# Kernel tuning notes

Hardware: AMD Instinct MI355X
Metric: run time of the kernel (lower is better)

## Reference

```python
import jax, jax.numpy as jnp
import numpy as np

RADIUS = 10  # watermark_radius
EPS = 1e-5   # BatchNorm eps

def _conv(x, w, b, g, be, m, v):
    # Conv2d 3x3 pad 1 + BatchNorm(eval) + ReLU, NCHW
    y = jax.lax.conv_general_dilated(x, w, (1, 1), 'SAME',
                                     dimension_numbers=('NCHW', 'OIHW', 'NCHW'))
    y = y + b[None, :, None, None]
    y = g[None, :, None, None] * (y - m[None, :, None, None]) * jax.lax.rsqrt(v + EPS)[None, :, None, None] + be[None, :, None, None]
    return jax.nn.relu(y)

def _watermark_indices(C, H, W, L, r):
    # Replicates the (channel, i, j) iteration order of the torch loop.
    chs, ys, xs = [], [], []
    cy0, cx0 = H // 2, W // 2
    for c in range(C):
        for i in range(-r, r + 1):
            for j in range(-r, r + 1):
                if len(chs) >= L:
                    return np.array(chs), np.array(ys), np.array(xs)
                y, x = cy0 + i, cx0 + j
                if 0 <= y < H and 0 <= x < W and i * i + j * j <= r * r:
                    chs.append(c); ys.append(y); xs.append(x)
    return np.array(chs), np.array(ys), np.array(xs)

def setup_inputs() -> dict:
    key = jax.random.key(0)
    ks = jax.random.split(key, 8)
    B, Cc, H, W, L = 16, 64, 256, 256, 256
    s = 0.05  # weight scale for numerical stability
    inp = {
        'image': jax.random.normal(ks[0], (B, 3, H, W), jnp.float32),
        'message': jax.random.uniform(ks[1], (B, L), jnp.float32),
        'w0': jax.random.normal(ks[2], (Cc, 3, 3, 3), jnp.float32) * s,
        'b0': jnp.zeros((Cc,), jnp.float32),
        'g0': jnp.ones((Cc,), jnp.float32),
        'be0': jnp.zeros((Cc,), jnp.float32),
        'm0': jnp.zeros((Cc,), jnp.float32),
        'v0': jnp.ones((Cc,), jnp.float32),
        'wk': jax.random.normal(ks[3], (3, Cc, Cc, 3, 3), jnp.float32) * s,
        'bk': jnp.zeros((3, Cc), jnp.float32),
        'gk': jnp.ones((3, Cc), jnp.float32),
        'bek': jnp.zeros((3, Cc), jnp.float32),
        'mk': jnp.zeros((3, Cc), jnp.float32),
        'vk': jnp.ones((3, Cc), jnp.float32),
        'wa': jax.random.normal(ks[4], (Cc, Cc + 3 + L, 3, 3), jnp.float32) * s,
        'ba': jnp.zeros((Cc,), jnp.float32),
        'ga': jnp.ones((Cc,), jnp.float32),
        'bea': jnp.zeros((Cc,), jnp.float32),
        'ma': jnp.zeros((Cc,), jnp.float32),
        'va': jnp.ones((Cc,), jnp.float32),
        'wf': jax.random.normal(ks[5], (3, Cc, 1, 1), jnp.float32) * s,
        'bf': jnp.zeros((3,), jnp.float32),
    }
    return inp

def reference(image, message, w0, b0, g0, be0, m0, v0,
              wk, bk, gk, bek, mk, vk,
              wa, ba, ga, bea, ma, va, wf, bf):
    B, _, H, W = image.shape
    L = message.shape[1]
    # conv stack
    x = _conv(image, w0, b0, g0, be0, m0, v0)
    for t in range(wk.shape[0]):
        x = _conv(x, wk[t], bk[t], gk[t], bek[t], mk[t], vk[t])
    C = x.shape[1]
    # FFT2 over spatial dims
    fft = jnp.fft.fft2(x.astype(jnp.complex64))
    # vectorized tree-ring watermark scatter (precomputed static indices)
    ch, yy, xx = _watermark_indices(C, H, W, L, RADIUS)
    vals = message[:, :ch.shape[0]]                      # [B, L]
    cvals = (vals + 1j * vals).astype(jnp.complex64)     # complex(value, value)
    fft = fft.at[:, ch, yy, xx].set(cvals)
    enc = jnp.fft.ifft2(fft).real.astype(image.dtype)
    # concat [expanded message, encoded, image]
    msg = jnp.broadcast_to(message[:, :, None, None], (B, L, H, W))
    cat = jnp.concatenate([msg, enc, image], axis=1)
    y = _conv(cat, wa, ba, ga, bea, ma, va)
    # final 1x1 conv
    out = jnp.einsum('bchw,oc->bohw', y, wf[:, :, 0, 0]) + bf[None, :, None, None]
    return out
```

## Files before the change

kernel.cpp:

```cpp
#include <hip/hip_runtime.h>
#include <hip/hip_bf16.h>

#define HH 256
#define WW 256
#define NB 16
#define CC 64
#define NL 256
#define HWSZ (HH*WW)
#define EPSV 1e-5f
#define CAST 104
#define NYK 16
#define YK0 118

using bf16 = __hip_bfloat16;
using short8  = __attribute__((ext_vector_type(8))) short;
using floatx4 = __attribute__((ext_vector_type(4))) float;

__device__ __forceinline__ ushort f2b(float f){
    bf16 h = __float2bfloat16(f);
    union { bf16 h; ushort u; } cv; cv.h = h; return cv.u;
}
__device__ __forceinline__ float b2fu(ushort u){
    union { unsigned int i; float f; } cv; cv.i = ((unsigned int)u) << 16; return cv.f;
}

__global__ void prep_w_k(const float* __restrict__ wk, const float* __restrict__ wa,
                         ushort* __restrict__ wkb2, ushort* __restrict__ wab2)
{
    int i = blockIdx.x*256 + threadIdx.x;
    const int NWK = 3*9*64*64, NWA = 9*64*96;
    if (i < NWK) {
        int ci8 = i & 7; int r = i >> 3;
        int lane = r & 63; r >>= 6;
        int mi = r & 3; r >>= 2;
        int g = r % 18; int t = r / 18;
        int q = g / 6, kc2 = (g / 3) & 1, p = g % 3;
        int quad = lane >> 4, n16 = lane & 15;
        int co = mi*16 + n16, ci = kc2*32 + quad*8 + ci8, tap = p*3 + q;
        wkb2[i] = f2b(wk[(((size_t)t*64 + co)*64 + ci)*9 + tap]);
    } else if (i < NWK + NWA) {
        int i2 = i - NWK;
        int ci8 = i2 & 7; int r = i2 >> 3;
        int lane = r & 63; r >>= 6;
        int mi = r & 3; r >>= 2;
        int g = r;
        int q = g / 9, kc3 = (g / 3) % 3, p = g % 3;
        int quad = lane >> 4, n16 = lane & 15;
        int co = mi*16 + n16, ci = kc3*32 + quad*8 + ci8, tap = p*3 + q;
        float v = 0.f;
        if (ci < 64)      v = wa[((size_t)co*323 + 256 + ci)*9 + tap];
        else if (ci < 67) v = wa[((size_t)co*323 + 320 + (ci-64))*9 + tap];
        wab2[i2] = f2b(v);
    }
}

#define LDAF(DST, G) { const ushort* bp = wbase + (size_t)(G)*2048;            \
    _Pragma("unroll") for (int mi_=0; mi_<4; mi_++)                            \
        DST[mi_] = *(const short8*)(bp + mi_*512); }

#define MFMA_GRP(AF, BF, P)                                                    \
    _Pragma("unroll") for (int mi_=0; mi_<4; mi_++) {                          \
      _Pragma("unroll") for (int ni_=0; ni_<4; ni_++)                          \
        acc[mi_][ni_] = __builtin_amdgcn_mfma_f32_16x16x32_bf16(               \
            AF[mi_], BF[ni_+(P)], acc[mi_][ni_], 0, 0, 0); }

__global__ __launch_bounds__(256) void conv0_k(
    const float* __restrict__ img, const float* __restrict__ w0,
    const float* __restrict__ bias, const float* __restrict__ gamma,
    const float* __restrict__ beta, const float* __restrict__ mean,
    const float* __restrict__ var, ushort* __restrict__ outp)
{
    __shared__ float s_i[3][18][18];
    __shared__ float s_wv[64*27];
    __shared__ float s_al[64], s_be[64];
    __shared__ ushort __align__(16) s_y[256*72];

    int tid = threadIdx.x;
    int x0 = blockIdx.x*16, y0 = blockIdx.y*16, b = blockIdx.z;
    if (tid < 64) {
        float a = gamma[tid]*rsqrtf(var[tid]+EPSV);
        s_al[tid] = a; s_be[tid] = (bias[tid]-mean[tid])*a + beta[tid];
    }
    for (int c = tid; c < 64*27; c += 256) s_wv[c] = w0[c];
    for (int c = tid; c < 3*18*18; c += 256) {
        int ci = c / 324, pp = c % 324, py = pp/18, px = pp%18;
        int gy = y0-1+py, gx = x0-1+px;
        float v = 0.f;
        if ((unsigned)gy < 256u && (unsigned)gx < 256u)
            v = img[((size_t)b*3 + ci)*HWSZ + gy*256 + gx];
        s_i[ci][py][px] = v;
    }
    __syncthreads();

    int ly = tid >> 4, lx = tid & 15;
    float xv[27];
    #pragma unroll
    for (int ci=0;ci<3;ci++)
      #pragma unroll
      for (int p=0;p<3;p++)
        #pragma unroll
        for (int q=0;q<3;q++)
            xv[ci*9+p*3+q] = s_i[ci][ly+p][lx+q];

    for (int co=0; co<64; co++) {
        float a = 0.f;
        #pragma unroll
        for (int j=0;j<27;j++) a += xv[j]*s_wv[co*27+j];
        s_y[tid*72 + co] = f2b(fmaxf(s_al[co]*a + s_be[co], 0.f));
    }
    __syncthreads();
    size_t obase = (size_t)b*HWSZ*64;
    for (int c = tid; c < 256*8; c += 256) {
        int ci8 = c & 7, px = c >> 3;
        int gy = y0 + (px>>4), gx = x0 + (px&15);
        *(uint4*)&outp[obase + (size_t)(gy*256+gx)*64 + ci8*8] =
            *(const uint4*)&s_y[px*72 + ci8*8];
    }
}

__global__ __launch_bounds__(256,3) void convm_k(
    const ushort* __restrict__ in, const ushort* __restrict__ wgt,
    ushort* __restrict__ outp,
    const float* __restrict__ gamma, const float* __restrict__ beta,
    const float* __restrict__ mean,  const float* __restrict__ var,
    const float* __restrict__ bias,  float* __restrict__ plane)
{
    __shared__ ushort __align__(16) s_x[18*18*72];
    __shared__ float s_al[64], s_be[64];

    const int tid = threadIdx.x;
    const int x0 = blockIdx.x*16, y0 = blockIdx.y*16, b = blockIdx.z;

    if (tid < 64) {
        float a = gamma[tid]*rsqrtf(var[tid]+EPSV);
        s_al[tid] = a; s_be[tid] = (bias[tid]-mean[tid])*a + beta[tid];
    }
    const size_t ibase = (size_t)b*HWSZ*64;
    for (int c = tid; c < 18*18*8; c += 256) {
        int ci8 = c & 7, pp = c >> 3;
        int px = pp % 18, py = pp / 18;
        int gy = y0-1+py, gx = x0-1+px;
        uint4 v = make_uint4(0,0,0,0);
        if ((unsigned)gy < 256u && (unsigned)gx < 256u)
            v = *(const uint4*)&in[ibase + (size_t)(gy*256+gx)*64 + ci8*8];
        *(uint4*)&s_x[(py*18+px)*72 + ci8*8] = v;
    }
    __syncthreads();

    const int lane = tid & 63, wid = tid >> 6;
    const int n16 = lane & 15, quad = lane >> 4;
    const ushort* wbase = wgt + (size_t)lane*8;

    floatx4 acc[4][4];
    #pragma unroll
    for (int mi=0;mi<4;mi++)
      #pragma unroll
      for (int ni=0;ni<4;ni++)
        #pragma unroll
        for (int r=0;r<4;r++) acc[mi][ni][r] = 0.f;

    short8 afA[4], afB[4], bfA[6], bfB[6];

    LDAF(afA, 0);
    #pragma unroll
    for (int rr=0; rr<6; rr++)
        bfA[rr] = *(const short8*)&s_x[((wid*4+rr)*18 + n16)*72 + quad*8];

    #pragma unroll
    for (int g=0; g<18; g++) {
        const int p = g % 3, j = g / 3;
        if (g+1 < 18) {
            if (g & 1) { LDAF(afA, g+1); } else { LDAF(afB, g+1); }
        }
        if (p == 0 && j+1 < 6) {
            const int nq = (j+1) >> 1, nk = (j+1) & 1;
            if (j & 1) {
                #pragma unroll
                for (int rr=0; rr<6; rr++)
                    bfA[rr] = *(const short8*)&s_x[((wid*4+rr)*18 + n16 + nq)*72 + nk*32 + quad*8];
            } else {
                #pragma unroll
                for (int rr=0; rr<6; rr++)
                    bfB[rr] = *(const short8*)&s_x[((wid*4+rr)*18 + n16 + nq)*72 + nk*32 + quad*8];
            }
        }
        if (g & 1) { if (j & 1) { MFMA_GRP(afB, bfB, p) } else { MFMA_GRP(afB, bfA, p) } }
        else       { if (j & 1) { MFMA_GRP(afA, bfB, p) } else { MFMA_GRP(afA, bfA, p) } }
    }
    __syncthreads();

    ushort* s_y = s_x;
    #pragma unroll
    for (int mi=0;mi<4;mi++)
      #pragma unroll
      for (int ni=0;ni<4;ni++) {
        int px = (wid*4+ni)*16 + n16;
        int cob = mi*16 + quad*4;
        ushort u[4];
        #pragma unroll
        for (int r=0;r<4;r++) {
            float y = fmaxf(s_al[cob+r]*acc[mi][ni][r] + s_be[cob+r], 0.f);
            u[r] = f2b(y);
            if (plane && mi==0 && quad==0 && r==0)
                plane[(size_t)b*HWSZ + (y0+wid*4+ni)*256 + x0 + n16] = y;
        }
        uint2 pk; pk.x = (uint)u[0] | ((uint)u[1]<<16); pk.y = (uint)u[2] | ((uint)u[3]<<16);
        *(uint2*)&s_y[px*72 + cob] = pk;
      }
    __syncthreads();
    for (int c = tid; c < 256*8; c += 256) {
        int ci8 = c & 7, px = c >> 3;
        int gy = y0 + (px>>4), gx = x0 + (px&15);
        *(uint4*)&outp[ibase + (size_t)(gy*256+gx)*64 + ci8*8] =
            *(const uint4*)&s_y[px*72 + ci8*8];
    }
}

__global__ __launch_bounds__(256,2) void conva_k(
    const ushort* __restrict__ enc, const float* __restrict__ img,
    const float* __restrict__ dplane, const ushort* __restrict__ wgt,
    const float* __restrict__ gamma, const float* __restrict__ beta,
    const float* __restrict__ mean,  const float* __restrict__ var,
    const float* __restrict__ bias,
    const float* __restrict__ Tb,
    const float* __restrict__ wf, const float* __restrict__ bfv,
    float* __restrict__ outp)
{
    __shared__ ushort __align__(16) s_x[18*18*CAST];
    __shared__ float s_al[64], s_be[64];
    __shared__ float s_T[64*9];
    __shared__ float s_wf[3*64];
    __shared__ float s_bf[3];

    const int tid = threadIdx.x;
    const int x0 = blockIdx.x*16, y0 = blockIdx.y*16, b = blockIdx.z;

    if (tid < 64) {
        float a = gamma[tid]*rsqrtf(var[tid]+EPSV);
        s_al[tid] = a; s_be[tid] = (bias[tid]-mean[tid])*a + beta[tid];
    }
    if (tid < 192) s_wf[tid] = wf[tid];
    if (tid < 3)   s_bf[tid] = bfv[tid];
    for (int c = tid; c < 64*9; c += 256) s_T[c] = Tb[(size_t)b*576 + c];

    const size_t ibase = (size_t)b*HWSZ*64;
    for (int c = tid; c < 18*18*8; c += 256) {
        int ci8 = c & 7, pp = c >> 3;
        int px = pp % 18, py = pp / 18;
        int gy = y0-1+py, gx = x0-1+px;
        uint4 v = make_uint4(0,0,0,0);
        if ((unsigned)gy < 256u && (unsigned)gx < 256u) {
            v = *(const uint4*)&enc[ibase + (size_t)(gy*256+gx)*64 + ci8*8];
            if (ci8 == 0) {
                float d = dplane[(size_t)b*HWSZ + gy*256 + gx];
                ushort nb = f2b(b2fu((ushort)(v.x & 0xffffu)) + d);
                v.x = (v.x & 0xffff0000u) | (uint)nb;
            }
        }
        *(uint4*)&s_x[(py*18+px)*CAST + ci8*8] = v;
    }
    for (int c = tid; c < 18*18*5; c += 256) {
        int ci8 = 8 + c % 5, pp = c / 5;
        int px = pp % 18, py = pp / 18;
        int gy = y0-1+py, gx = x0-1+px;
        uint4 v = make_uint4(0,0,0,0);
        if (ci8 == 8 && (unsigned)gy < 256u && (unsigned)gx < 256u) {
            float i0 = img[((size_t)b*3 + 0)*HWSZ + gy*256 + gx];
            float i1 = img[((size_t)b*3 + 1)*HWSZ + gy*256 + gx];
            float i2 = img[((size_t)b*3 + 2)*HWSZ + gy*256 + gx];
            v.x = (uint)f2b(i0) | ((uint)f2b(i1) << 16);
            v.y = (uint)f2b(i2);
        }
        *(uint4*)&s_x[(py*18+px)*CAST + ci8*8] = v;
    }
    __syncthreads();

    const int lane = tid & 63, wid = tid >> 6;
    const int n16 = lane & 15, quad = lane >> 4;
    const ushort* wbase = wgt + (size_t)lane*8;

    floatx4 acc[4][4];
    #pragma unroll
    for (int mi=0;mi<4;mi++)
      #pragma unroll
      for (int ni=0;ni<4;ni++)
        #pragma unroll
        for (int r=0;r<4;r++) acc[mi][ni][r] = 0.f;

    short8 afA[4], afB[4], bfA[6], bfB[6];

    LDAF(afA, 0);
    #pragma unroll
    for (int rr=0; rr<6; rr++)
        bfA[rr] = *(const short8*)&s_x[((wid*4+rr)*18 + n16)*CAST + quad*8];

    #pragma unroll
    for (int g=0; g<27; g++) {
        const int p = g % 3, j = g / 3;
        if (g+1 < 27) {
            if (g & 1) { LDAF(afA, g+1); } else { LDAF(afB, g+1); }
        }
        if (p == 0 && j+1 < 9) {
            const int nq = (j+1) / 3, nk = (j+1) % 3;
            if (j & 1) {
                #pragma unroll
                for (int rr=0; rr<6; rr++)
                    bfA[rr] = *(const short8*)&s_x[((wid*4+rr)*18 + n16 + nq)*CAST + nk*32 + quad*8];
            } else {
                #pragma unroll
                for (int rr=0; rr<6; rr++)
                    bfB[rr] = *(const short8*)&s_x[((wid*4+rr)*18 + n16 + nq)*CAST + nk*32 + quad*8];
            }
        }
        if (g & 1) { if (j & 1) { MFMA_GRP(afB, bfB, p) } else { MFMA_GRP(afB, bfA, p) } }
        else       { if (j & 1) { MFMA_GRP(afA, bfB, p) } else { MFMA_GRP(afA, bfA, p) } }
    }

    float po[3][4];
    #pragma unroll
    for (int o=0;o<3;o++)
      #pragma unroll
      for (int ni=0;ni<4;ni++) po[o][ni] = 0.f;

    #pragma unroll
    for (int mi=0;mi<4;mi++) {
        int cob = mi*16 + quad*4;
        #pragma unroll
        for (int r=0;r<4;r++) {
            int co = cob + r;
            float al = s_al[co], be = s_be[co];
            const float* t = &s_T[co*9];
            float w0f = s_wf[0*64+co], w1f = s_wf[1*64+co], w2f = s_wf[2*64+co];
            #pragma unroll
            for (int ni=0;ni<4;ni++) {
                int h = y0 + wid*4 + ni, w = x0 + n16;
                float tv = t[0];
                if (h==0)   tv -= t[1];
                if (h==255) tv -= t[2];
                if (w==0)   tv -= t[3];
                if (w==255) tv -= t[4];
                if (h==0   && w==0)   tv += t[5];
                if (h==0   && w==255) tv += t[6];
                if (h==255 && w==0)   tv += t[7];
                if (h==255 && w==255) tv += t[8];
                float y = fmaxf(al*(acc[mi][ni][r] + tv) + be, 0.f);
                po[0][ni] += w0f*y; po[1][ni] += w1f*y; po[2][ni] += w2f*y;
            }
        }
    }
    #pragma unroll
    for (int o=0;o<3;o++)
      #pragma unroll
      for (int ni=0;ni<4;ni++) {
        float pv = po[o][ni];
        pv += __shfl_xor(pv, 16, 64);
        pv += __shfl_xor(pv, 32, 64);
        if (quad == o) {
            int h = y0 + wid*4 + ni, w = x0 + n16;
            outp[((size_t)b*3 + o)*HWSZ + h*256 + w] = pv + s_bf[o];
        }
      }
}

__global__ __launch_bounds__(256) void msgterm_k(const float* __restrict__ msg,
                                                 const float* __restrict__ wa,
                                                 float* __restrict__ Tbuf)
{
    __shared__ float red[256];
    int b = blockIdx.x, o = blockIdx.y, l = threadIdx.x;
    float m = msg[b*NL + l];
    float wv[9];
    #pragma unroll
    for (int t=0;t<9;t++) wv[t] = wa[((size_t)o*323 + l)*9 + t] * m;
    float comp[9];
    comp[0] = wv[0]+wv[1]+wv[2]+wv[3]+wv[4]+wv[5]+wv[6]+wv[7]+wv[8];
    comp[1] = wv[0]+wv[1]+wv[2];
    comp[2] = wv[6]+wv[7]+wv[8];
    comp[3] = wv[0]+wv[3]+wv[6];
    comp[4] = wv[2]+wv[5]+wv[8];
    comp[5] = wv[0]; comp[6]=wv[2]; comp[7]=wv[6]; comp[8]=wv[8];
    for (int cpi=0;cpi<9;cpi++){
        red[l] = comp[cpi];
        __syncthreads();
        for (int s=128;s>0;s>>=1){ if (l<s) red[l]+=red[l+s]; __syncthreads(); }
        if (l==0) Tbuf[((size_t)b*CC+o)*9+cpi] = red[0];
        __syncthreads();
    }
}

__global__ void build_idx_k(int* __restrict__ idx)
{
    if (threadIdx.x==0 && blockIdx.x==0) {
        int n=0;
        for (int i=-10;i<=10;i++)
            for (int j=-10;j<=10;j++) {
                if (n>=NL) return;
                if (i*i+j*j<=100) { idx[2*n]=128+i; idx[2*n+1]=128+j; n++; }
            }
    }
}

__global__ __launch_bounds__(256) void colA_k(const float* __restrict__ plane,
                                              float* __restrict__ Cbuf)
{
    __shared__ float twc[256], tws[256];
    int t = blockIdx.x, b = blockIdx.y, w = threadIdx.x;
    float sv, cv;
    __sincosf(6.283185307179586f * (float)w / 256.0f, &sv, &cv);
    twc[w]=cv; tws[w]=sv;
    __syncthreads();
    int yk = YK0 + t;
    const float* pb = &plane[(size_t)b*HWSZ];
    int m = 0;
    float fr=0.f, fi=0.f;
    for (int h=0; h<256; h++) {
        float xv = pb[h*256 + w];
        fr += xv*twc[m];
        fi -= xv*tws[m];
        m = (m + yk) & 255;
    }
    float* Cb = &Cbuf[((size_t)(b*NYK + t)*2)*256];
    Cb[w]       = fr;
    Cb[256 + w] = fi;
}

__global__ __launch_bounds__(256) void freqB_k(const float* __restrict__ Cbuf,
                                               const float* __restrict__ msg,
                                               const int* __restrict__ idx,
                                               float* __restrict__ D)
{
    __shared__ float twc[256], tws[256];
    __shared__ float sfr[4], sfi[4];
    int k = blockIdx.x, b = blockIdx.y, w = threadIdx.x;
    float sv, cv;
    __sincosf(6.283185307179586f * (float)w / 256.0f, &sv, &cv);
    twc[w]=cv; tws[w]=sv;
    __syncthreads();
    int yk = idx[2*k], xk = idx[2*k+1];
    int t = yk - YK0;
    const float* Cb = &Cbuf[((size_t)(b*NYK + t)*2)*256];
    float Cr = Cb[w], Ci = Cb[256 + w];
    int ang = (xk*w) & 255;
    float cx = twc[ang], sx = tws[ang];
    float fr = Cr*cx + Ci*sx;
    float fi = Ci*cx - Cr*sx;
    #pragma unroll
    for (int off=32; off>0; off>>=1) {
        fr += __shfl_xor(fr, off, 64);
        fi += __shfl_xor(fi, off, 64);
    }
    if ((w & 63) == 0) { sfr[w>>6] = fr; sfi[w>>6] = fi; }
    __syncthreads();
    if (w == 0) {
        float FR = sfr[0]+sfr[1]+sfr[2]+sfr[3];
        float FI = sfi[0]+sfi[1]+sfi[2]+sfi[3];
        float mv = msg[b*NL + k];
        D[((size_t)b*NL + k)*2 + 0] = mv - FR;
        D[((size_t)b*NL + k)*2 + 1] = mv - FI;
    }
}

__global__ __launch_bounds__(256) void rowC_k(const int* __restrict__ idx,
                                              const float* __restrict__ D,
                                              float* __restrict__ Sbuf)
{
    __shared__ float twc[256], tws[256], dr[256], di[256];
    __shared__ int iy[256], ix[256];
    int t = blockIdx.x, b = blockIdx.y, w = threadIdx.x;
    float sv, cv;
    __sincosf(6.283185307179586f * (float)w / 256.0f, &sv, &cv);
    twc[w]=cv; tws[w]=sv;
    dr[w] = D[((size_t)b*NL + w)*2+0];
    di[w] = D[((size_t)b*NL + w)*2+1];
    iy[w] = idx[2*w]; ix[w] = idx[2*w+1];
    __syncthreads();
    int yk = YK0 + t;
    float Sr=0.f, Si=0.f;
    for (int k=0;k<256;k++) {
        if (iy[k] != yk) continue;
        int ang = (ix[k]*w) & 255;
        float c = twc[ang], s = tws[ang];
        Sr += dr[k]*c - di[k]*s;
        Si += dr[k]*s + di[k]*c;
    }
    float* Sb = &Sbuf[((size_t)(b*NYK + t)*2)*256];
    Sb[w]       = Sr;
    Sb[256 + w] = Si;
}

__global__ __launch_bounds__(256) void applyD_k(const float* __restrict__ Sbuf,
                                                float* __restrict__ dplane)
{
    __shared__ float twc[256], tws[256];
    int h = blockIdx.x, b = blockIdx.y, w = threadIdx.x;
    float sv, cv;
    __sincosf(6.283185307179586f * (float)w / 256.0f, &sv, &cv);
    twc[w]=cv; tws[w]=sv;
    __syncthreads();
    float acc = 0.f;
    #pragma unroll
    for (int t=0;t<NYK;t++) {
        int yk = YK0 + t;
        int ang = (yk*h) & 255;
        float cy = twc[ang], sy = tws[ang];
        const float* Sb = &Sbuf[((size_t)(b*NYK + t)*2)*256];
        acc += cy*Sb[w] - sy*Sb[256 + w];
    }
    dplane[(size_t)b*HWSZ + h*256 + w] = acc * (1.0f/65536.0f);
}

extern "C" void kernel_launch(void* const* d_in, const int* in_sizes, int n_in,
                              void* d_out, int out_size, void* d_ws, size_t ws_size,
                              hipStream_t stream)
{
    const float* image = (const float*)d_in[0];
    const float* msg   = (const float*)d_in[1];
    const float* w0    = (const float*)d_in[2];
    const float* b0    = (const float*)d_in[3];
    const float* g0    = (const float*)d_in[4];
    const float* be0   = (const float*)d_in[5];
    const float* m0    = (const float*)d_in[6];
    const float* v0    = (const float*)d_in[7];
    const float* wk    = (const float*)d_in[8];
    const float* bk    = (const float*)d_in[9];
    const float* gk    = (const float*)d_in[10];
    const float* bek   = (const float*)d_in[11];
    const float* mk    = (const float*)d_in[12];
    const float* vk    = (const float*)d_in[13];
    const float* wa    = (const float*)d_in[14];
    const float* ba    = (const float*)d_in[15];
    const float* ga    = (const float*)d_in[16];
    const float* bea   = (const float*)d_in[17];
    const float* ma    = (const float*)d_in[18];
    const float* va    = (const float*)d_in[19];
    const float* wf    = (const float*)d_in[20];
    const float* bfv   = (const float*)d_in[21];
    float* out = (float*)d_out;

    char* base = (char*)d_ws;
    int*    idx    = (int*)base;
    float*  Dbuf   = (float*)(base + (4<<10));
    float*  Tbuf   = (float*)(base + (40<<10));
    ushort* wkb2   = (ushort*)(base + (128<<10));
    ushort* wab2   = (ushort*)(base + (384<<10));
    float*  Cbuf   = (float*)(base + (512<<10));
    float*  Sbuf   = (float*)(base + ((size_t)1<<20));
    float*  plane  = (float*)(base + ((size_t)2<<20));
    float*  dplane = (float*)(base + ((size_t)7<<20));
    ushort* bufA   = (ushort*)(base + ((size_t)12<<20));

    const size_t perB = (size_t)HWSZ*64*2*2;
    int chunk = 1;
    for (int c = NB; c >= 1; c >>= 1)
        if (((size_t)12<<20) + (size_t)c*perB <= ws_size) { chunk = c; break; }
    ushort* bufB = bufA + (size_t)chunk*HWSZ*64;

    build_idx_k<<<1,64,0,stream>>>(idx);
    msgterm_k<<<dim3(NB,CC),256,0,stream>>>(msg, wa, Tbuf);
    int prep_n = (3*9*64*64 + 9*64*96 + 255)/256;
    prep_w_k<<<prep_n,256,0,stream>>>(wk, wa, wkb2, wab2);

    const size_t WL = (size_t)9*64*64;

    for (int cs = 0; cs < NB; cs += chunk) {
        dim3 g(16,16,chunk);
        const float* img_c = image + (size_t)cs*3*HWSZ;

        conv0_k<<<g,256,0,stream>>>(img_c, w0, b0, g0, be0, m0, v0, bufA);
        convm_k<<<g,256,0,stream>>>(bufA, wkb2 + 0*WL, bufB,
            gk+0*CC, bek+0*CC, mk+0*CC, vk+0*CC, bk+0*CC, nullptr);
        convm_k<<<g,256,0,stream>>>(bufB, wkb2 + 1*WL, bufA,
            gk+1*CC, bek+1*CC, mk+1*CC, vk+1*CC, bk+1*CC, nullptr);
        convm_k<<<g,256,0,stream>>>(bufA, wkb2 + 2*WL, bufB,
            gk+2*CC, bek+2*CC, mk+2*CC, vk+2*CC, bk+2*CC, plane);

        colA_k<<<dim3(NYK,chunk),256,0,stream>>>(plane, Cbuf);
        freqB_k<<<dim3(NL,chunk),256,0,stream>>>(Cbuf, msg + (size_t)cs*NL, idx, Dbuf);
        rowC_k<<<dim3(NYK,chunk),256,0,stream>>>(idx, Dbuf, Sbuf);
        applyD_k<<<dim3(HH,chunk),256,0,stream>>>(Sbuf, dplane);

        conva_k<<<g,256,0,stream>>>(bufB, img_c, dplane, wab2,
            ga, bea, ma, va, ba, Tbuf + (size_t)cs*CC*9, wf, bfv,
            out + (size_t)cs*3*HWSZ);
    }
}
```

Baseline: 885.4 us.

## Fold image channels into a single im2col MFMA step in final conv

The final conv previously padded the input to 96 channels (64 encoded plus 3 image channels plus zeros) and ran 27 MFMA groups. It now runs 18 groups over the 64 encoded channels and handles the 3 image channels as one im2col K=32 group (27 taps packed), loaded directly from global into registers. The weight layout is repacked to match, shared memory shrinks from 104 to 72 channels per pixel, and launch bounds are raised to 3 blocks per CU. This removes padded MFMA work and LDS use, at the cost of scattered global image loads per thread and more register pressure.

New measurement: 926.6 us. +4.7%, slower.

```diff
diff --git a/kernel.cpp b/kernel.cpp
--- a/kernel.cpp
+++ b/kernel.cpp
@@ -8,7 +8,6 @@
 #define NL 256
 #define HWSZ (HH*WW)
 #define EPSV 1e-5f
-#define CAST 104
 #define NYK 16
 #define YK0 118
 
@@ -28,7 +27,7 @@
                          ushort* __restrict__ wkb2, ushort* __restrict__ wab2)
 {
     int i = blockIdx.x*256 + threadIdx.x;
-    const int NWK = 3*9*64*64, NWA = 9*64*96;
+    const int NWK = 3*9*64*64, NWA = 19*2048;
     if (i < NWK) {
         int ci8 = i & 7; int r = i >> 3;
         int lane = r & 63; r >>= 6;
@@ -42,14 +41,21 @@
         int i2 = i - NWK;
         int ci8 = i2 & 7; int r = i2 >> 3;
         int lane = r & 63; r >>= 6;
-        int mi = r & 3; r >>= 2;
-        int g = r;
-        int q = g / 9, kc3 = (g / 3) % 3, p = g % 3;
+        int mi = r & 3; int g = r >> 2;
         int quad = lane >> 4, n16 = lane & 15;
-        int co = mi*16 + n16, ci = kc3*32 + quad*8 + ci8, tap = p*3 + q;
+        int co = mi*16 + n16;
         float v = 0.f;
-        if (ci < 64)      v = wa[((size_t)co*323 + 256 + ci)*9 + tap];
-        else if (ci < 67) v = wa[((size_t)co*323 + 320 + (ci-64))*9 + tap];
+        if (g < 18) {
+            int q = g/6, kc2 = (g/3)&1, p = g%3;
+            int ci = kc2*32 + quad*8 + ci8, tap = p*3 + q;
+            v = wa[((size_t)co*323 + 256 + ci)*9 + tap];
+        } else {
+            int j = quad*8 + ci8;
+            if (j < 27) {
+                int ci = j/9, rem = j%9;
+                v = wa[((size_t)co*323 + 320 + ci)*9 + rem];
+            }
+        }
         wab2[i2] = f2b(v);
     }
 }
@@ -216,7 +222,7 @@
     }
 }
 
-__global__ __launch_bounds__(256,2) void conva_k(
+__global__ __launch_bounds__(256,3) void conva_k(
     const ushort* __restrict__ enc, const float* __restrict__ img,
     const float* __restrict__ dplane, const ushort* __restrict__ wgt,
     const float* __restrict__ gamma, const float* __restrict__ beta,
@@ -226,7 +232,7 @@
     const float* __restrict__ wf, const float* __restrict__ bfv,
     float* __restrict__ outp)
 {
-    __shared__ ushort __align__(16) s_x[18*18*CAST];
+    __shared__ ushort __align__(16) s_x[18*18*72];
     __shared__ float s_al[64], s_be[64];
     __shared__ float s_T[64*9];
     __shared__ float s_wf[3*64];
@@ -242,6 +248,10 @@
     if (tid < 192) s_wf[tid] = wf[tid];
     if (tid < 3)   s_bf[tid] = bfv[tid];
     for (int c = tid; c < 64*9; c += 256) s_T[c] = Tb[(size_t)b*576 + c];
+
+    const int lane = tid & 63, wid = tid >> 6;
+    const int n16 = lane & 15, quad = lane >> 4;
+    const ushort* wbase = wgt + (size_t)lane*8;
 
     const size_t ibase = (size_t)b*HWSZ*64;
     for (int c = tid; c < 18*18*8; c += 256) {
@@ -257,27 +267,28 @@
                 v.x = (v.x & 0xffff0000u) | (uint)nb;
             }
         }
-        *(uint4*)&s_x[(py*18+px)*CAST + ci8*8] = v;
-    }
-    for (int c = tid; c < 18*18*5; c += 256) {
-        int ci8 = 8 + c % 5, pp = c / 5;
-        int px = pp % 18, py = pp / 18;
-        int gy = y0-1+py, gx = x0-1+px;
-        uint4 v = make_uint4(0,0,0,0);
-        if (ci8 == 8 && (unsigned)gy < 256u && (unsigned)gx < 256u) {
-            float i0 = img[((size_t)b*3 + 0)*HWSZ + gy*256 + gx];
-            float i1 = img[((size_t)b*3 + 1)*HWSZ + gy*256 + gx];
-            float i2 = img[((size_t)b*3 + 2)*HWSZ + gy*256 + gx];
-            v.x = (uint)f2b(i0) | ((uint)f2b(i1) << 16);
-            v.y = (uint)f2b(i2);
-        }
-        *(uint4*)&s_x[(py*18+px)*CAST + ci8*8] = v;
-    }
-    __syncthreads();
-
-    const int lane = tid & 63, wid = tid >> 6;
-    const int n16 = lane & 15, quad = lane >> 4;
-    const ushort* wbase = wgt + (size_t)lane*8;
+        *(uint4*)&s_x[(py*18+px)*72 + ci8*8] = v;
+    }
+
+    short8 bimg[4];
+    #pragma unroll
+    for (int ni=0; ni<4; ni++) {
+        short8 t;
+        #pragma unroll
+        for (int ci8=0; ci8<8; ci8++) {
+            int j = quad*8 + ci8;
+            float v = 0.f;
+            if (j < 27) {
+                int ci = j/9, rem = j%9, p = rem/3, q = rem%3;
+                int gy = y0 + wid*4 + ni + p - 1, gx = x0 + n16 + q - 1;
+                if ((unsigned)gy < 256u && (unsigned)gx < 256u)
+                    v = img[((size_t)b*3 + ci)*HWSZ + gy*256 + gx];
+            }
+            t[ci8] = (short)f2b(v);
+        }
+        bimg[ni] = t;
+    }
+    __syncthreads();
 
     floatx4 acc[4][4];
     #pragma unroll
@@ -287,34 +298,27 @@
         #pragma unroll
         for (int r=0;r<4;r++) acc[mi][ni][r] = 0.f;
 
-    short8 afA[4], afB[4], bfA[6], bfB[6];
+    short8 afA[4], afB[4], bf[6];
 
     LDAF(afA, 0);
     #pragma unroll
-    for (int rr=0; rr<6; rr++)
-        bfA[rr] = *(const short8*)&s_x[((wid*4+rr)*18 + n16)*CAST + quad*8];
-
-    #pragma unroll
-    for (int g=0; g<27; g++) {
+    for (int g=0; g<18; g++) {
         const int p = g % 3, j = g / 3;
-        if (g+1 < 27) {
-            if (g & 1) { LDAF(afA, g+1); } else { LDAF(afB, g+1); }
-        }
-        if (p == 0 && j+1 < 9) {
-            const int nq = (j+1) / 3, nk = (j+1) % 3;
-            if (j & 1) {
-                #pragma unroll
-                for (int rr=0; rr<6; rr++)
-                    bfA[rr] = *(const short8*)&s_x[((wid*4+rr)*18 + n16 + nq)*CAST + nk*32 + quad*8];
-            } else {
-                #pragma unroll
-                for (int rr=0; rr<6; rr++)
-                    bfB[rr] = *(const short8*)&s_x[((wid*4+rr)*18 + n16 + nq)*CAST + nk*32 + quad*8];
-            }
-        }
-        if (g & 1) { if (j & 1) { MFMA_GRP(afB, bfB, p) } else { MFMA_GRP(afB, bfA, p) } }
-        else       { if (j & 1) { MFMA_GRP(afA, bfB, p) } else { MFMA_GRP(afA, bfA, p) } }
-    }
+        if (g & 1) { LDAF(afA, g+1); } else { LDAF(afB, g+1); }
+        if (p == 0) {
+            const int nq = j >> 1, nk = j & 1;
+            #pragma unroll
+            for (int rr=0; rr<6; rr++)
+                bf[rr] = *(const short8*)&s_x[((wid*4+rr)*18 + n16 + nq)*72 + nk*32 + quad*8];
+        }
+        if (g & 1) { MFMA_GRP(afB, bf, p) } else { MFMA_GRP(afA, bf, p) }
+    }
+    #pragma unroll
+    for (int mi=0;mi<4;mi++)
+      #pragma unroll
+      for (int ni=0;ni<4;ni++)
+        acc[mi][ni] = __builtin_amdgcn_mfma_f32_16x16x32_bf16(
+            afA[mi], bimg[ni], acc[mi][ni], 0, 0, 0);
 
     float po[3][4];
     #pragma unroll
@@ -557,7 +561,7 @@
 
     build_idx_k<<<1,64,0,stream>>>(idx);
     msgterm_k<<<dim3(NB,CC),256,0,stream>>>(msg, wa, Tbuf);
-    int prep_n = (3*9*64*64 + 9*64*96 + 255)/256;
+    int prep_n = (3*9*64*64 + 19*2048 + 255)/256;
     prep_w_k<<<prep_n,256,0,stream>>>(wk, wa, wkb2, wab2);
 
     const size_t WL = (size_t)9*64*64;
```
